# Performance work log

Measured on AMD Instinct MI355X. Metric: run time of the kernel, lower is better.

The kernel has to match this reference:

```python
import jax, jax.numpy as jnp
import numpy as np

NUM_GROUPS = 8   # also the per-group channel count (C = NUM_GROUPS**2)
NUM_LEVELS = 4
RADIUS = 4


def setup_inputs() -> dict:
    key = jax.random.key(0)
    k1, k2, k3 = jax.random.split(key, 3)
    B, C, H, W = 2, 64, 80, 160
    fmap1 = jax.random.normal(k1, (B, C, H, W), dtype=jnp.float32)
    fmap2 = jax.random.normal(k2, (B, C, H, W), dtype=jnp.float32)
    coords = jax.random.uniform(k3, (B, 1, H, W), dtype=jnp.float32) * (W - 1)
    return {"fmap1": fmap1, "fmap2": fmap2, "coords": coords}


def _build_cost_volume(fmap1, fmap2):
    # group-wise correlation: torch.split(fmap, G, dim=1) -> chunks of G channels
    B, C, H, W = fmap1.shape
    G = NUM_GROUPS
    gc = NUM_GROUPS  # chunk size; C == G * gc
    f1 = fmap1.reshape(B, G, gc, H, W)
    f2 = fmap2.reshape(B, G, gc, H, W)
    # cv[b,g,h,w,v] = sum_c f1[b,g,c,h,w] * f2[b,g,c,h,v] / sqrt(gc)
    cv = jnp.einsum('bgchw,bgchv->bghwv', f1, f2) / jnp.sqrt(jnp.float32(gc))
    return cv  # (B, G, H, W, W2)


def _pyramid(cv, n_levels):
    pyr = [cv]
    for _ in range(n_levels):
        B, G, H, W, Wl = cv.shape
        cv = cv.reshape(B, G, H, W, Wl // 2, 2).mean(-1)  # avg_pool1d(k=2,s=2)
        pyr.append(cv)
    return pyr


def _linear_sample(cv, x):
    # cv: (B,G,H,W,Wl) 1D signals; x: (B,G,H,W,K) sample positions
    Wl = cv.shape[-1]
    x0 = jnp.floor(x)
    w1 = x - x0
    i0 = x0.astype(jnp.int32)
    i1 = i0 + 1
    g0 = jnp.take_along_axis(cv, jnp.clip(i0, 0, Wl - 1), axis=-1)
    g1 = jnp.take_along_axis(cv, jnp.clip(i1, 0, Wl - 1), axis=-1)
    v0 = (i0 >= 0) & (i0 < Wl)
    v1 = (i1 >= 0) & (i1 < Wl)
    zero = jnp.zeros((), cv.dtype)
    return jnp.where(v0, g0 * (1.0 - w1), zero) + jnp.where(v1, g1 * w1, zero)


def reference(fmap1, fmap2, coords):
    B, _, H, W = coords.shape
    G, r = NUM_GROUPS, RADIUS
    K = 2 * r + 1
    cv = _build_cost_volume(fmap1, fmap2)
    geo = cv  # regularizer_3d treated as identity (see notes)
    feat_pyr = _pyramid(cv, NUM_LEVELS)
    geo_pyr = _pyramid(geo, NUM_LEVELS)
    dx = jnp.linspace(-r, r, K, dtype=jnp.float32)  # (K,)
    c = coords[:, 0][:, None]  # (B,1,H,W), broadcasts over groups
    outs = []
    for i in range(NUM_LEVELS):
        coords_lvl = c[..., None] / (2.0 ** i) + dx  # (B,1,H,W,K)
        coords_lvl = jnp.broadcast_to(coords_lvl, (B, G, H, W, K))
        for pyr in (feat_pyr, geo_pyr):
            s = _linear_sample(pyr[i], coords_lvl)            # (B,G,H,W,K)
            outs.append(s.transpose(0, 2, 3, 1, 4).reshape(B, H, W, G * K))
    out = jnp.concatenate(outs, axis=-1)  # (B,H,W, 2*L*G*K)
    return out.transpose(0, 3, 1, 2).astype(jnp.float32)
```

## Files before the change

### kernel.cpp

```cpp
#include <hip/hip_runtime.h>
#include <hip/hip_fp16.h>


namespace {
constexpr int B_ = 2, C_ = 64, H_ = 80, W_ = 160;
constexpr int G_ = 8, GC_ = 8, L_ = 4, K_ = 9, R_ = 4;
constexpr int HW_ = H_ * W_;
constexpr int NCH_ = 2 * L_ * G_ * K_;
constexpr int TPB = 320;
constexpr int NBINS = 160 + 80 + 40 + 20;
constexpr float INV_SQRT_GC = 0.35355339059327373f;
}

__global__ __launch_bounds__(TPB) void gacv_kernel(
    const float* __restrict__ fmap1, const float* __restrict__ fmap2,
    const float* __restrict__ coords, float* __restrict__ out) {
  __shared__ __half2 pln[4][NBINS];

  const int tid = threadIdx.x;
  const int bid = blockIdx.x;
  const int half = bid & 1;
  const int rid = bid >> 1;
  const int h = rid % H_;
  const int bg = rid / H_;
  const int g = bg % G_;
  const int b = bg / G_;

  const float* f2base = fmap2 + (size_t)(b * C_ + g * GC_) * HW_ + h * W_;
  for (int idx = tid; idx < 4 * W_; idx += TPB) {
    int v = idx % W_;
    int pair = idx / W_;
    float lo = f2base[(2 * pair) * HW_ + v];
    float hi = f2base[(2 * pair + 1) * HW_ + v];
    pln[pair][v] = __floats2half2_rn(lo, hi);
  }
  __syncthreads();
  const __half2 halfc = __float2half2_rn(0.5f);
  {
    int t = tid % 80, pair = tid / 80;
    pln[pair][160 + t] = __hmul2(__hadd2(pln[pair][2 * t], pln[pair][2 * t + 1]), halfc);
  }
  __syncthreads();
  if (tid < 160) {
    int t = tid % 40, pair = tid / 40;
    pln[pair][240 + t] = __hmul2(__hadd2(pln[pair][160 + 2 * t], pln[pair][160 + 2 * t + 1]), halfc);
  }
  __syncthreads();
  if (tid < 80) {
    int t = tid % 20, pair = tid / 20;
    pln[pair][280 + t] = __hmul2(__hadd2(pln[pair][240 + 2 * t], pln[pair][240 + 2 * t + 1]), halfc);
  }
  __syncthreads();

  const int w_local = tid % 80;
  const int lvl = tid / 80;
  const int w = half * 80 + w_local;

  float f1v[GC_];
  const float* f1base = fmap1 + (size_t)(b * C_ + g * GC_) * HW_ + h * W_ + w;
#pragma unroll
  for (int c = 0; c < GC_; ++c) f1v[c] = f1base[c * HW_] * INV_SQRT_GC;

  const float cx = coords[(b * H_ + h) * W_ + w];
  const float xl = ldexpf(cx, -lvl);
  const int Wl = W_ >> lvl;
  const int ofs = 320 - (320 >> lvl);
  const float F = floorf(xl);
  const int fi = (int)F;
  const float w1 = xl - F;
  const float w0 = 1.0f - w1;

  float T[2 * R_ + 2];
#pragma unroll
  for (int j = 0; j < 2 * R_ + 2; ++j) {
    int t = fi - R_ + j;
    int tc = min(max(t, 0), Wl - 1);
    int bi = ofs + tc;
    float2 c0 = __half22float2(pln[0][bi]);
    float2 c1 = __half22float2(pln[1][bi]);
    float2 c2 = __half22float2(pln[2][bi]);
    float2 c3 = __half22float2(pln[3][bi]);
    float s = f1v[0] * c0.x + f1v[1] * c0.y + f1v[2] * c1.x + f1v[3] * c1.y +
              f1v[4] * c2.x + f1v[5] * c2.y + f1v[6] * c3.x + f1v[7] * c3.y;
    T[j] = (t == tc) ? s : 0.0f;
  }

  float* outb = out + (size_t)b * NCH_ * HW_ + h * W_ + w;
  const int chBase = lvl * (2 * G_ * K_) + g * K_;
#pragma unroll
  for (int k = 0; k < K_; ++k) {
    float val = w0 * T[k] + w1 * T[k + 1];
    outb[(size_t)(chBase + k) * HW_] = val;
    outb[(size_t)(chBase + G_ * K_ + k) * HW_] = val;
  }
}

extern "C" void kernel_launch(void* const* d_in, const int* in_sizes, int n_in,
                              void* d_out, int out_size, void* d_ws, size_t ws_size,
                              hipStream_t stream) {
  const float* fmap1 = (const float*)d_in[0];
  const float* fmap2 = (const float*)d_in[1];
  const float* coords = (const float*)d_in[2];
  float* out = (float*)d_out;
  gacv_kernel<<<dim3(B_ * G_ * H_ * 2), dim3(TPB), 0, stream>>>(fmap1, fmap2, coords, out);
}
```

Measured before the change: 85.44 us.

## Process two rows per block with four pixels per thread and float4 stores

Each block now handles two full image rows, not half a row. The fmap2 row planes and their pyramid are built once per row instead of twice, which removes the duplicated shared-memory setup. Each thread computes four adjacent pixels, so fmap1, coords and output traffic use 128-bit vectorized loads and stores. The cost is a 4x smaller grid (640 blocks), more registers per thread, and possibly lower occupancy or latency hiding.

```diff
diff --git a/kernel.cpp b/kernel.cpp
--- a/kernel.cpp
+++ b/kernel.cpp
@@ -15,83 +15,118 @@
 __global__ __launch_bounds__(TPB) void gacv_kernel(
     const float* __restrict__ fmap1, const float* __restrict__ fmap2,
     const float* __restrict__ coords, float* __restrict__ out) {
-  __shared__ __half2 pln[4][NBINS];
+  __shared__ __half2 pln[2][4][NBINS];
 
   const int tid = threadIdx.x;
   const int bid = blockIdx.x;
-  const int half = bid & 1;
-  const int rid = bid >> 1;
-  const int h = rid % H_;
-  const int bg = rid / H_;
+  const int hb = bid % (H_ / 2);
+  const int bg = bid / (H_ / 2);
   const int g = bg % G_;
   const int b = bg / G_;
+  const int h0 = 2 * hb;
 
-  const float* f2base = fmap2 + (size_t)(b * C_ + g * GC_) * HW_ + h * W_;
-  for (int idx = tid; idx < 4 * W_; idx += TPB) {
+  const float* f2base = fmap2 + (size_t)(b * C_ + g * GC_) * HW_ + h0 * W_;
+  for (int idx = tid; idx < 2 * 4 * W_; idx += TPB) {
     int v = idx % W_;
-    int pair = idx / W_;
-    float lo = f2base[(2 * pair) * HW_ + v];
-    float hi = f2base[(2 * pair + 1) * HW_ + v];
-    pln[pair][v] = __floats2half2_rn(lo, hi);
+    int r = idx / W_;
+    int pair = r & 3;
+    int hh = r >> 2;
+    float lo = f2base[(2 * pair) * HW_ + hh * W_ + v];
+    float hi = f2base[(2 * pair + 1) * HW_ + hh * W_ + v];
+    pln[hh][pair][v] = __floats2half2_rn(lo, hi);
   }
   __syncthreads();
   const __half2 halfc = __float2half2_rn(0.5f);
-  {
-    int t = tid % 80, pair = tid / 80;
-    pln[pair][160 + t] = __hmul2(__hadd2(pln[pair][2 * t], pln[pair][2 * t + 1]), halfc);
+  for (int idx = tid; idx < 2 * 4 * 80; idx += TPB) {
+    int t = idx % 80; int r = idx / 80; int pair = r & 3; int hh = r >> 2;
+    pln[hh][pair][160 + t] =
+        __hmul2(__hadd2(pln[hh][pair][2 * t], pln[hh][pair][2 * t + 1]), halfc);
   }
   __syncthreads();
-  if (tid < 160) {
-    int t = tid % 40, pair = tid / 40;
-    pln[pair][240 + t] = __hmul2(__hadd2(pln[pair][160 + 2 * t], pln[pair][160 + 2 * t + 1]), halfc);
+  for (int idx = tid; idx < 2 * 4 * 40; idx += TPB) {
+    int t = idx % 40; int r = idx / 40; int pair = r & 3; int hh = r >> 2;
+    pln[hh][pair][240 + t] =
+        __hmul2(__hadd2(pln[hh][pair][160 + 2 * t], pln[hh][pair][160 + 2 * t + 1]), halfc);
   }
   __syncthreads();
-  if (tid < 80) {
-    int t = tid % 20, pair = tid / 20;
-    pln[pair][280 + t] = __hmul2(__hadd2(pln[pair][240 + 2 * t], pln[pair][240 + 2 * t + 1]), halfc);
+  for (int idx = tid; idx < 2 * 4 * 20; idx += TPB) {
+    int t = idx % 20; int r = idx / 20; int pair = r & 3; int hh = r >> 2;
+    pln[hh][pair][280 + t] =
+        __hmul2(__hadd2(pln[hh][pair][240 + 2 * t], pln[hh][pair][240 + 2 * t + 1]), halfc);
   }
   __syncthreads();
 
-  const int w_local = tid % 80;
-  const int lvl = tid / 80;
-  const int w = half * 80 + w_local;
+  const int w4 = tid % 40;
+  const int rl = tid / 40;
+  const int lvl = rl & 3;
+  const int hh = rl >> 2;
+  const int h = h0 + hh;
 
-  float f1v[GC_];
-  const float* f1base = fmap1 + (size_t)(b * C_ + g * GC_) * HW_ + h * W_ + w;
-#pragma unroll
-  for (int c = 0; c < GC_; ++c) f1v[c] = f1base[c * HW_] * INV_SQRT_GC;
-
-  const float cx = coords[(b * H_ + h) * W_ + w];
-  const float xl = ldexpf(cx, -lvl);
+  const float lscale = __int_as_float(0x3f800000 - (lvl << 23));
   const int Wl = W_ >> lvl;
   const int ofs = 320 - (320 >> lvl);
-  const float F = floorf(xl);
-  const int fi = (int)F;
-  const float w1 = xl - F;
-  const float w0 = 1.0f - w1;
 
-  float T[2 * R_ + 2];
+  float4 f1m[GC_];
+  const float* f1base = fmap1 + (size_t)(b * C_ + g * GC_) * HW_ + h * W_ + 4 * w4;
 #pragma unroll
-  for (int j = 0; j < 2 * R_ + 2; ++j) {
-    int t = fi - R_ + j;
-    int tc = min(max(t, 0), Wl - 1);
-    int bi = ofs + tc;
-    float2 c0 = __half22float2(pln[0][bi]);
-    float2 c1 = __half22float2(pln[1][bi]);
-    float2 c2 = __half22float2(pln[2][bi]);
-    float2 c3 = __half22float2(pln[3][bi]);
-    float s = f1v[0] * c0.x + f1v[1] * c0.y + f1v[2] * c1.x + f1v[3] * c1.y +
-              f1v[4] * c2.x + f1v[5] * c2.y + f1v[6] * c3.x + f1v[7] * c3.y;
-    T[j] = (t == tc) ? s : 0.0f;
+  for (int c = 0; c < GC_; ++c) {
+    float4 v = *(const float4*)(f1base + c * HW_);
+    f1m[c] = make_float4(v.x * INV_SQRT_GC, v.y * INV_SQRT_GC,
+                         v.z * INV_SQRT_GC, v.w * INV_SQRT_GC);
+  }
+  const float4 cx4 = *(const float4*)(coords + (b * H_ + h) * W_ + 4 * w4);
+
+  float4 vals[K_];
+#pragma unroll
+  for (int p = 0; p < 4; ++p) {
+    const float cx = (p == 0) ? cx4.x : (p == 1) ? cx4.y : (p == 2) ? cx4.z : cx4.w;
+    const float xl = cx * lscale;
+    const float F = floorf(xl);
+    const int fi = (int)F;
+    const float w1 = xl - F;
+    const float w0 = 1.0f - w1;
+
+    float T[2 * R_ + 2];
+#pragma unroll
+    for (int j = 0; j < 2 * R_ + 2; ++j) {
+      int t = fi - R_ + j;
+      int tc = min(max(t, 0), Wl - 1);
+      int bi = ofs + tc;
+      float2 c0 = __half22float2(pln[hh][0][bi]);
+      float2 c1 = __half22float2(pln[hh][1][bi]);
+      float2 c2 = __half22float2(pln[hh][2][bi]);
+      float2 c3 = __half22float2(pln[hh][3][bi]);
+      float s;
+      if (p == 0)
+        s = f1m[0].x * c0.x + f1m[1].x * c0.y + f1m[2].x * c1.x + f1m[3].x * c1.y +
+            f1m[4].x * c2.x + f1m[5].x * c2.y + f1m[6].x * c3.x + f1m[7].x * c3.y;
+      else if (p == 1)
+        s = f1m[0].y * c0.x + f1m[1].y * c0.y + f1m[2].y * c1.x + f1m[3].y * c1.y +
+            f1m[4].y * c2.x + f1m[5].y * c2.y + f1m[6].y * c3.x + f1m[7].y * c3.y;
+      else if (p == 2)
+        s = f1m[0].z * c0.x + f1m[1].z * c0.y + f1m[2].z * c1.x + f1m[3].z * c1.y +
+            f1m[4].z * c2.x + f1m[5].z * c2.y + f1m[6].z * c3.x + f1m[7].z * c3.y;
+      else
+        s = f1m[0].w * c0.x + f1m[1].w * c0.y + f1m[2].w * c1.x + f1m[3].w * c1.y +
+            f1m[4].w * c2.x + f1m[5].w * c2.y + f1m[6].w * c3.x + f1m[7].w * c3.y;
+      T[j] = (t == tc) ? s : 0.0f;
+    }
+#pragma unroll
+    for (int k = 0; k < K_; ++k) {
+      float v = w0 * T[k] + w1 * T[k + 1];
+      if (p == 0) vals[k].x = v;
+      else if (p == 1) vals[k].y = v;
+      else if (p == 2) vals[k].z = v;
+      else vals[k].w = v;
+    }
   }
 
-  float* outb = out + (size_t)b * NCH_ * HW_ + h * W_ + w;
+  float4* outb4 = (float4*)out + (size_t)b * NCH_ * (HW_ / 4) + (h * W_) / 4 + w4;
   const int chBase = lvl * (2 * G_ * K_) + g * K_;
 #pragma unroll
   for (int k = 0; k < K_; ++k) {
-    float val = w0 * T[k] + w1 * T[k + 1];
-    outb[(size_t)(chBase + k) * HW_] = val;
-    outb[(size_t)(chBase + G_ * K_ + k) * HW_] = val;
+    outb4[(size_t)(chBase + k) * (HW_ / 4)] = vals[k];
+    outb4[(size_t)(chBase + G_ * K_ + k) * (HW_ / 4)] = vals[k];
   }
 }
 
@@ -102,5 +137,5 @@
   const float* fmap2 = (const float*)d_in[1];
   const float* coords = (const float*)d_in[2];
   float* out = (float*)d_out;
-  gacv_kernel<<<dim3(B_ * G_ * H_ * 2), dim3(TPB), 0, stream>>>(fmap1, fmap2, coords, out);
+  gacv_kernel<<<dim3(B_ * G_ * (H_ / 2)), dim3(TPB), 0, stream>>>(fmap1, fmap2, coords, out);
 }
```

Result: slower. 89.28 us (+4.5%).
